# Performance work log

Measured on AMD Instinct MI355X. Metric: run time of the kernel, lower is better.

## Reference

```python
import jax, jax.numpy as jnp
import numpy as np

B, C, D, H, W = 2, 128, 16, 16, 16
NH = 4
HD = C // NH
GROUPS = 32
EPS = 1e-5


def group_norm(x, w, b):
    # x: [B, C, D, H, W]; normalize over (C/GROUPS, D, H, W) per group
    Bb, Cc = x.shape[0], x.shape[1]
    xr = x.reshape(Bb, GROUPS, -1)
    mu = xr.mean(axis=-1, keepdims=True)
    var = xr.var(axis=-1, keepdims=True)
    xn = ((xr - mu) * jax.lax.rsqrt(var + EPS)).reshape(x.shape)
    return xn * w.reshape(1, Cc, 1, 1, 1) + b.reshape(1, Cc, 1, 1, 1)


def setup_inputs() -> dict:
    key = jax.random.key(0)
    k0, k1, k2 = jax.random.split(key, 3)
    x = jax.random.normal(k0, (B, C, D, H, W), dtype=jnp.float32)
    gn_w = jnp.ones((C,), dtype=jnp.float32)
    gn_b = jnp.zeros((C,), dtype=jnp.float32)
    # 1x1x1 Conv3d weights as [out_ch, in_ch] matrices
    qkv_w = jax.random.normal(k1, (3 * C, C), dtype=jnp.float32) / np.sqrt(C).astype(np.float32)
    qkv_b = jnp.zeros((3 * C,), dtype=jnp.float32)
    out_w = jax.random.normal(k2, (C, C), dtype=jnp.float32) / np.sqrt(C).astype(np.float32)
    out_b = jnp.zeros((C,), dtype=jnp.float32)
    return {"x": x, "gn_w": gn_w, "gn_b": gn_b, "qkv_w": qkv_w, "qkv_b": qkv_b,
            "out_w": out_w, "out_b": out_b}


def reference(x, gn_w, gn_b, qkv_w, qkv_b, out_w, out_b):
    Bb, Cc, Dd, Hh, Ww = x.shape
    N = Dd * Hh * Ww
    scale = HD ** (-0.5)

    xn = group_norm(x, gn_w, gn_b)
    xf = xn.reshape(Bb, Cc, N)                              # [B, C, N]
    qkv = jnp.einsum('oc,bcn->bon', qkv_w, xf) + qkv_b[None, :, None]
    qkv = qkv.reshape(Bb, 3, NH, HD, N)
    q, k, v = qkv[:, 0], qkv[:, 1], qkv[:, 2]               # each [B, h, hd, N]

    attn = jnp.einsum('bhdn,bhdm->bhnm', q, k) * scale      # [B, h, N, N]
    attn = jax.nn.softmax(attn, axis=-1)
    o = jnp.einsum('bhnm,bhdm->bhdn', attn, v)              # [B, h, hd, N]
    o = o.reshape(Bb, Cc, N)

    y = jnp.einsum('oc,bcn->bon', out_w, o) + out_b[None, :, None]
    return y.reshape(Bb, Cc, Dd, Hh, Ww) + x
```

## Files before the change

### kernel.cpp

```cpp
#include <hip/hip_runtime.h>
#include <hip/hip_bf16.h>

#define B_ 2
#define C_ 128
#define N_ 4096
#define NH_ 4
#define HD_ 32
#define GROUPS_ 32
#define EPS_ 1e-5f
#define SCALE2_ 0.25503486f
#define NCH_ 4
#define CHKV_ 1024
#define NT_ (CHKV_ / 64)

typedef __attribute__((ext_vector_type(2))) float f32x2;
typedef __attribute__((ext_vector_type(4))) float f32x4;
typedef __attribute__((ext_vector_type(8))) short s16x8;
typedef __attribute__((ext_vector_type(2))) unsigned int u32x2;
typedef __attribute__((ext_vector_type(4))) unsigned int u32x4;
typedef unsigned short u16;
typedef unsigned int u32;

static __device__ __forceinline__ u32 cvtpk_bf16(float lo, float hi) {
  u32 r;
  asm("v_cvt_pk_bf16_f32 %0, %1, %2" : "=v"(r) : "v"(lo), "v"(hi));
  return r;
}
static __device__ __forceinline__ float fexp2(float x) {
  float r;
  asm("v_exp_f32 %0, %1" : "=v"(r) : "v"(x));
  return r;
}
static __device__ __forceinline__ float bflo(u32 w) { return __uint_as_float(w << 16); }
static __device__ __forceinline__ float bfhi(u32 w) { return __uint_as_float(w & 0xffff0000u); }

__global__ __launch_bounds__(256) void k_groupnorm(
    const float* __restrict__ x, const float* __restrict__ gw,
    const float* __restrict__ gb, u16* __restrict__ xn) {
  const int blk = blockIdx.x;
  const int tid = threadIdx.x;
  const size_t base = (size_t)blk * (4 * N_);
  const f32x4* x4 = (const f32x4*)(x + base);
  float s = 0.f, ss = 0.f;
  for (int i = tid; i < 4096; i += 256) {
    f32x4 v = x4[i];
    s  += v.x + v.y + v.z + v.w;
    ss += v.x*v.x + v.y*v.y + v.z*v.z + v.w*v.w;
  }
  for (int off = 32; off; off >>= 1) {
    s  += __shfl_down(s, off);
    ss += __shfl_down(ss, off);
  }
  __shared__ float red[2][4];
  __shared__ float mv[2];
  const int wid = tid >> 6;
  if ((tid & 63) == 0) { red[0][wid] = s; red[1][wid] = ss; }
  __syncthreads();
  if (tid == 0) {
    float S = red[0][0]+red[0][1]+red[0][2]+red[0][3];
    float Q = red[1][0]+red[1][1]+red[1][2]+red[1][3];
    float mu  = S * (1.f/16384.f);
    float var = Q * (1.f/16384.f) - mu*mu;
    mv[0] = mu; mv[1] = rsqrtf(var + EPS_);
  }
  __syncthreads();
  const float mu = mv[0], rs = mv[1];
  const int gi = blk & (GROUPS_ - 1);
  u32x2* xn2 = (u32x2*)(xn + base);
  for (int i = tid; i < 4096; i += 256) {
    const int c = gi*4 + (i >> 10);
    const float a  = gw[c] * rs;
    const float b2 = gb[c] - mu * a;
    f32x4 v = x4[i];
    f32x4 r = v * a + b2;
    u32x2 p = { cvtpk_bf16(r.x, r.y), cvtpk_bf16(r.z, r.w) };
    xn2[i] = p;
  }
}

__global__ __launch_bounds__(256) void k_gemm_qkv(
    const u16* __restrict__ xn, const float* __restrict__ w,
    const float* __restrict__ bias, u16* __restrict__ qkvb,
    u16* __restrict__ Kt) {
  const int tid = threadIdx.x;
  const int n0 = blockIdx.x * 512 + tid * 2;
  const int o0 = blockIdx.y * 8;
  const int b  = blockIdx.z;
  const u16* xb = xn + (size_t)b * C_ * N_;
  const float* wp = w + (size_t)o0 * C_;
  float ax[8] = {0,0,0,0,0,0,0,0};
  float ay[8] = {0,0,0,0,0,0,0,0};
  #pragma unroll 4
  for (int c = 0; c < C_; ++c) {
    const u32 wv = *(const u32*)(xb + (size_t)c * N_ + n0);
    const float x0 = bflo(wv), x1 = bfhi(wv);
    #pragma unroll
    for (int i = 0; i < 8; ++i) {
      const float wi = wp[(size_t)i * C_ + c];
      ax[i] += x0 * wi;
      ay[i] += x1 * wi;
    }
  }
  #pragma unroll
  for (int i = 0; i < 8; ++i) {
    const float bi = bias[o0 + i];
    ax[i] += bi; ay[i] += bi;
  }
  if (o0 < 128) {
    u16* op = qkvb + ((size_t)b * 384 + o0) * N_ + n0;
    #pragma unroll
    for (int i = 0; i < 8; ++i)
      *(u32*)(op + (size_t)i * N_) = cvtpk_bf16(ax[i] * SCALE2_, ay[i] * SCALE2_);
  } else if (o0 < 256) {
    const int h  = (o0 - 128) >> 5;
    const int d8 = (o0 - 128) & 31;
    u16* kb = Kt + (size_t)(b * NH_ + h) * N_ * HD_ + d8;
    u32x4 pk0 = { cvtpk_bf16(ax[0], ax[1]), cvtpk_bf16(ax[2], ax[3]),
                  cvtpk_bf16(ax[4], ax[5]), cvtpk_bf16(ax[6], ax[7]) };
    u32x4 pk1 = { cvtpk_bf16(ay[0], ay[1]), cvtpk_bf16(ay[2], ay[3]),
                  cvtpk_bf16(ay[4], ay[5]), cvtpk_bf16(ay[6], ay[7]) };
    *(u32x4*)(kb + (size_t)n0 * HD_)       = pk0;
    *(u32x4*)(kb + (size_t)(n0 + 1) * HD_) = pk1;
  } else {
    u16* op = qkvb + ((size_t)b * 384 + o0) * N_ + n0;
    #pragma unroll
    for (int i = 0; i < 8; ++i)
      *(u32*)(op + (size_t)i * N_) = cvtpk_bf16(ax[i], ay[i]);
  }
}

__global__ __launch_bounds__(256) void k_attn(
    const u16* __restrict__ qkvb, const u16* __restrict__ Kt,
    float* __restrict__ Opart, float* __restrict__ Lpart) {
  __shared__ u16 Kl[64 * 32];
  __shared__ u16 Vl[32 * 72];
  const int b = blockIdx.z, h = blockIdx.y;
  const int qt = blockIdx.x & 31, ch = blockIdx.x >> 5;
  const int tid = threadIdx.x;
  const int wid = tid >> 6, lane = tid & 63;
  const int g = lane >> 4, lq = lane & 15;
  const int q0 = qt * 128 + wid * 16;
  const int kv0 = ch * CHKV_;

  const u16* qb = qkvb + ((size_t)b * 384 + h * HD_) * N_;
  s16x8 qfA, qfB;
  #pragma unroll
  for (int j = 0; j < 8; ++j) {
    qfA[j] = (short)qb[(size_t)(8*g + j) * N_ + q0 + lq];
    qfB[j] = (short)qb[(size_t)(8*g + j) * N_ + q0 + 64 + lq];
  }

  const u16* ktb = Kt + (size_t)(b * NH_ + h) * N_ * HD_;
  const u16* vbb = qkvb + ((size_t)b * 384 + 256 + h * HD_) * N_;
  const int pi = ((lq >> 2) << 3) + (lq & 3);

  const u16* kst = ktb + (size_t)kv0 * HD_ + tid * 8;
  const int vrow = tid >> 3;
  const int vcol = (tid & 7) * 8;
  const u16* vst = vbb + (size_t)vrow * N_ + kv0 + vcol;
  u16* kdst = Kl + ((tid * 8) ^ (((tid >> 5) & 3) * 8));
  u16* vdst = Vl + vrow * 72 + vcol;

  const int xsw  = (pi >> 3) & 3;
  const int slot = 8 * (g ^ xsw);
  const int ka0 = (pi)      * 32 + slot;
  const int ka1 = (pi + 4)  * 32 + slot;
  const int ka2 = (pi + 32) * 32 + slot;
  const int ka3 = (pi + 36) * 32 + slot;
  const int va0 = lq * 72 + 8*g;
  const int va1 = (lq + 16) * 72 + 8*g;

  const short one_bf = (short)0x3F80;
  const s16x8 onesB = {one_bf, one_bf, one_bf, one_bf,
                       one_bf, one_bf, one_bf, one_bf};

  f32x4 oa0A = {0.f,0.f,0.f,0.f}, oa1A = oa0A, oLA = oa0A;
  f32x4 oa0B = oa0A, oa1B = oa0A, oLB = oa0A;

  {
    s16x8 kr = *(const s16x8*)(kst);
    s16x8 vr = *(const s16x8*)(vst);
    *(s16x8*)(kdst) = kr;
    *(s16x8*)(vdst) = vr;
  }
  __syncthreads();

  for (int tt = 0; tt < NT_; ++tt) {
    const int tn = (tt + 1 < NT_) ? (tt + 1) : (NT_ - 1);
    s16x8 kr = *(const s16x8*)(kst + (size_t)tn * 64 * HD_);
    s16x8 vr = *(const s16x8*)(vst + (size_t)tn * 64);

    const s16x8 ck0 = *(const s16x8*)(Kl + ka0);
    const s16x8 ck1 = *(const s16x8*)(Kl + ka1);
    const s16x8 ck2 = *(const s16x8*)(Kl + ka2);
    const s16x8 ck3 = *(const s16x8*)(Kl + ka3);
    const s16x8 cv0 = *(const s16x8*)(Vl + va0);
    const s16x8 cv1 = *(const s16x8*)(Vl + va1);
    const s16x8 cv2 = *(const s16x8*)(Vl + va0 + 32);
    const s16x8 cv3 = *(const s16x8*)(Vl + va1 + 32);

    const f32x4 z = {0.f,0.f,0.f,0.f};
    {
      f32x4 s0 = __builtin_amdgcn_mfma_f32_16x16x32_bf16(ck0, qfA, z, 0, 0, 0);
      f32x4 s1 = __builtin_amdgcn_mfma_f32_16x16x32_bf16(ck1, qfA, z, 0, 0, 0);
      f32x4 s2 = __builtin_amdgcn_mfma_f32_16x16x32_bf16(ck2, qfA, z, 0, 0, 0);
      f32x4 s3 = __builtin_amdgcn_mfma_f32_16x16x32_bf16(ck3, qfA, z, 0, 0, 0);
      float p0 = fexp2(s0.x), p1 = fexp2(s0.y), p2 = fexp2(s0.z), p3 = fexp2(s0.w);
      float p4 = fexp2(s1.x), p5 = fexp2(s1.y), p6 = fexp2(s1.z), p7 = fexp2(s1.w);
      float p8 = fexp2(s2.x), p9 = fexp2(s2.y), pa_ = fexp2(s2.z), pb_ = fexp2(s2.w);
      float pc_ = fexp2(s3.x), pd_ = fexp2(s3.y), pe_ = fexp2(s3.z), pf_ = fexp2(s3.w);
      union { u32x4 u; s16x8 s; } pkA, pkB;
      pkA.u.x = cvtpk_bf16(p0, p1);   pkA.u.y = cvtpk_bf16(p2, p3);
      pkA.u.z = cvtpk_bf16(p4, p5);   pkA.u.w = cvtpk_bf16(p6, p7);
      pkB.u.x = cvtpk_bf16(p8, p9);   pkB.u.y = cvtpk_bf16(pa_, pb_);
      pkB.u.z = cvtpk_bf16(pc_, pd_); pkB.u.w = cvtpk_bf16(pe_, pf_);
      oa0A = __builtin_amdgcn_mfma_f32_16x16x32_bf16(pkA.s, cv0, oa0A, 0, 0, 0);
      oa1A = __builtin_amdgcn_mfma_f32_16x16x32_bf16(pkA.s, cv1, oa1A, 0, 0, 0);
      oLA  = __builtin_amdgcn_mfma_f32_16x16x32_bf16(pkA.s, onesB, oLA, 0, 0, 0);
      oa0A = __builtin_amdgcn_mfma_f32_16x16x32_bf16(pkB.s, cv2, oa0A, 0, 0, 0);
      oa1A = __builtin_amdgcn_mfma_f32_16x16x32_bf16(pkB.s, cv3, oa1A, 0, 0, 0);
      oLA  = __builtin_amdgcn_mfma_f32_16x16x32_bf16(pkB.s, onesB, oLA, 0, 0, 0);
    }
    {
      f32x4 s0 = __builtin_amdgcn_mfma_f32_16x16x32_bf16(ck0, qfB, z, 0, 0, 0);
      f32x4 s1 = __builtin_amdgcn_mfma_f32_16x16x32_bf16(ck1, qfB, z, 0, 0, 0);
      f32x4 s2 = __builtin_amdgcn_mfma_f32_16x16x32_bf16(ck2, qfB, z, 0, 0, 0);
      f32x4 s3 = __builtin_amdgcn_mfma_f32_16x16x32_bf16(ck3, qfB, z, 0, 0, 0);
      float p0 = fexp2(s0.x), p1 = fexp2(s0.y), p2 = fexp2(s0.z), p3 = fexp2(s0.w);
      float p4 = fexp2(s1.x), p5 = fexp2(s1.y), p6 = fexp2(s1.z), p7 = fexp2(s1.w);
      float p8 = fexp2(s2.x), p9 = fexp2(s2.y), pa_ = fexp2(s2.z), pb_ = fexp2(s2.w);
      float pc_ = fexp2(s3.x), pd_ = fexp2(s3.y), pe_ = fexp2(s3.z), pf_ = fexp2(s3.w);
      union { u32x4 u; s16x8 s; } pkA, pkB;
      pkA.u.x = cvtpk_bf16(p0, p1);   pkA.u.y = cvtpk_bf16(p2, p3);
      pkA.u.z = cvtpk_bf16(p4, p5);   pkA.u.w = cvtpk_bf16(p6, p7);
      pkB.u.x = cvtpk_bf16(p8, p9);   pkB.u.y = cvtpk_bf16(pa_, pb_);
      pkB.u.z = cvtpk_bf16(pc_, pd_); pkB.u.w = cvtpk_bf16(pe_, pf_);
      oa0B = __builtin_amdgcn_mfma_f32_16x16x32_bf16(pkA.s, cv0, oa0B, 0, 0, 0);
      oa1B = __builtin_amdgcn_mfma_f32_16x16x32_bf16(pkA.s, cv1, oa1B, 0, 0, 0);
      oLB  = __builtin_amdgcn_mfma_f32_16x16x32_bf16(pkA.s, onesB, oLB, 0, 0, 0);
      oa0B = __builtin_amdgcn_mfma_f32_16x16x32_bf16(pkB.s, cv2, oa0B, 0, 0, 0);
      oa1B = __builtin_amdgcn_mfma_f32_16x16x32_bf16(pkB.s, cv3, oa1B, 0, 0, 0);
      oLB  = __builtin_amdgcn_mfma_f32_16x16x32_bf16(pkB.s, onesB, oLB, 0, 0, 0);
    }

    __syncthreads();
    *(s16x8*)(kdst) = kr;
    *(s16x8*)(vdst) = vr;
    __syncthreads();
  }

  const int bh = b * NH_ + h;
  float* opb = Opart + ((size_t)ch * (B_ * NH_) + bh) * ((size_t)N_ * HD_);
  #pragma unroll
  for (int r = 0; r < 4; ++r) {
    const int qrow = q0 + g*4 + r;
    opb[(size_t)qrow * HD_ + lq]             = oa0A[r];
    opb[(size_t)qrow * HD_ + lq + 16]        = oa1A[r];
    opb[(size_t)(qrow + 64) * HD_ + lq]      = oa0B[r];
    opb[(size_t)(qrow + 64) * HD_ + lq + 16] = oa1B[r];
  }
  if (lq == 0) {
    float* lp = Lpart + ((size_t)ch * (B_ * NH_) + bh) * N_ + q0 + g*4;
    lp[0] = oLA[0]; lp[1] = oLA[1]; lp[2] = oLA[2]; lp[3] = oLA[3];
    lp[64] = oLB[0]; lp[65] = oLB[1]; lp[66] = oLB[2]; lp[67] = oLB[3];
  }
}

__global__ __launch_bounds__(256) void k_out(
    const float* __restrict__ Opart, const float* __restrict__ Lpart,
    const float* __restrict__ w, const float* __restrict__ bias,
    const float* __restrict__ x, float* __restrict__ y) {
  __shared__ u16 Ot[128][136];
  __shared__ float linv[NH_][128];
  const int t = threadIdx.x;
  const int n0 = blockIdx.x * 128;
  const int o0 = blockIdx.y * 16;
  const int b  = blockIdx.z;

  if (t < 128) {
    #pragma unroll
    for (int h = 0; h < NH_; ++h) {
      float s = 0.f;
      #pragma unroll
      for (int c = 0; c < NCH_; ++c)
        s += Lpart[((size_t)c * (B_ * NH_) + b * NH_ + h) * N_ + n0 + t];
      linv[h][t] = 1.0f / s;
    }
  }
  __syncthreads();

  {
    const int dd = (t & 7) * 4;
    const int nb = t >> 3;
    #pragma unroll
    for (int h = 0; h < NH_; ++h) {
      const float* ob = Opart + (size_t)(b * NH_ + h) * ((size_t)N_ * HD_)
                      + (size_t)n0 * HD_ + dd;
      #pragma unroll
      for (int p = 0; p < 4; ++p) {
        const int nn = p * 32 + nb;
        f32x4 a = {0.f,0.f,0.f,0.f};
        #pragma unroll
        for (int c = 0; c < NCH_; ++c)
          a += *(const f32x4*)(ob + (size_t)c * ((size_t)B_ * NH_ * N_ * HD_)
                                  + (size_t)nn * HD_);
        const float iv = linv[h][nn];
        a *= iv;
        Ot[32*h + dd + 0][nn] = (u16)cvtpk_bf16(a.x, a.x);
        Ot[32*h + dd + 1][nn] = (u16)cvtpk_bf16(a.y, a.y);
        Ot[32*h + dd + 2][nn] = (u16)cvtpk_bf16(a.z, a.z);
        Ot[32*h + dd + 3][nn] = (u16)cvtpk_bf16(a.w, a.w);
      }
    }
  }
  __syncthreads();

  const int n4  = (t & 31) * 4;
  const int orow = o0 + (t >> 5) * 2;
  const float* w0p = w + (size_t)orow * C_;
  const float* w1p = w0p + C_;
  f32x4 acc0 = {0.f,0.f,0.f,0.f}, acc1 = acc0;
  #pragma unroll 4
  for (int c = 0; c < C_; ++c) {
    const u32x2 ov = *(const u32x2*)(&Ot[c][n4]);
    const f32x4 xv = { bflo(ov.x), bfhi(ov.x), bflo(ov.y), bfhi(ov.y) };
    acc0 += xv * w0p[c];
    acc1 += xv * w1p[c];
  }
  const size_t yo = ((size_t)b * C_ + orow) * N_ + n0 + n4;
  const f32x4 xr0 = *(const f32x4*)(x + yo);
  const f32x4 xr1 = *(const f32x4*)(x + yo + N_);
  *(f32x4*)(y + yo)      = acc0 + bias[orow]     + xr0;
  *(f32x4*)(y + yo + N_) = acc1 + bias[orow + 1] + xr1;
}

extern "C" void kernel_launch(void* const* d_in, const int* in_sizes, int n_in,
                              void* d_out, int out_size, void* d_ws, size_t ws_size,
                              hipStream_t stream) {
  const float* x     = (const float*)d_in[0];
  const float* gn_w  = (const float*)d_in[1];
  const float* gn_b  = (const float*)d_in[2];
  const float* qkv_w = (const float*)d_in[3];
  const float* qkv_b = (const float*)d_in[4];
  const float* out_w = (const float*)d_in[5];
  const float* out_b = (const float*)d_in[6];
  float* y = (float*)d_out;

  float* ws  = (float*)d_ws;
  u16*   xn   = (u16*)ws;
  u16*   qkvb = (u16*)(ws + 524288);
  u16*   Kt   = (u16*)(ws + 2097152);
  float* Opart = ws + 2621440;
  float* Lpart = ws + 6815744;

  k_groupnorm<<<dim3(B_ * GROUPS_), 256, 0, stream>>>(x, gn_w, gn_b, xn);
  k_gemm_qkv <<<dim3(8, 48, B_),    256, 0, stream>>>(xn, qkv_w, qkv_b, qkvb, Kt);
  k_attn     <<<dim3(32 * NCH_, NH_, B_), 256, 0, stream>>>(qkvb, Kt, Opart, Lpart);
  k_out      <<<dim3(32, 8, B_),    256, 0, stream>>>(Opart, Lpart, out_w, out_b, x, y);
}
```

Before: 75.79 us.

## Split KV into more chunks, store bf16 partials, widen groupnorm and out-proj tiles

Doubles the number of KV chunks in attention (8 chunks of 512) to launch more blocks and use more CUs. Partial attention outputs are stored as bf16 instead of fp32, halving write and read traffic between attention and the output projection. Groupnorm now runs with 1024 threads per block, and the output projection computes 4 output rows per thread with half as many blocks, which improves weight reuse. In exchange, each query reduces over more partials, and bf16 rounding of those partials adds precision error.

```diff
diff --git a/kernel.cpp b/kernel.cpp
--- a/kernel.cpp
+++ b/kernel.cpp
@@ -9,8 +9,8 @@
 #define GROUPS_ 32
 #define EPS_ 1e-5f
 #define SCALE2_ 0.25503486f
-#define NCH_ 4
-#define CHKV_ 1024
+#define NCH_ 8
+#define CHKV_ 512
 #define NT_ (CHKV_ / 64)
 
 typedef __attribute__((ext_vector_type(2))) float f32x2;
@@ -33,8 +33,9 @@
 }
 static __device__ __forceinline__ float bflo(u32 w) { return __uint_as_float(w << 16); }
 static __device__ __forceinline__ float bfhi(u32 w) { return __uint_as_float(w & 0xffff0000u); }
-
-__global__ __launch_bounds__(256) void k_groupnorm(
+static __device__ __forceinline__ u16 f2bf16(float f) { return (u16)cvtpk_bf16(f, f); }
+
+__global__ __launch_bounds__(1024) void k_groupnorm(
     const float* __restrict__ x, const float* __restrict__ gw,
     const float* __restrict__ gb, u16* __restrict__ xn) {
   const int blk = blockIdx.x;
@@ -42,7 +43,8 @@
   const size_t base = (size_t)blk * (4 * N_);
   const f32x4* x4 = (const f32x4*)(x + base);
   float s = 0.f, ss = 0.f;
-  for (int i = tid; i < 4096; i += 256) {
+  #pragma unroll
+  for (int i = tid; i < 4096; i += 1024) {
     f32x4 v = x4[i];
     s  += v.x + v.y + v.z + v.w;
     ss += v.x*v.x + v.y*v.y + v.z*v.z + v.w*v.w;
@@ -51,14 +53,15 @@
     s  += __shfl_down(s, off);
     ss += __shfl_down(ss, off);
   }
-  __shared__ float red[2][4];
+  __shared__ float red[2][16];
   __shared__ float mv[2];
   const int wid = tid >> 6;
   if ((tid & 63) == 0) { red[0][wid] = s; red[1][wid] = ss; }
   __syncthreads();
   if (tid == 0) {
-    float S = red[0][0]+red[0][1]+red[0][2]+red[0][3];
-    float Q = red[1][0]+red[1][1]+red[1][2]+red[1][3];
+    float S = 0.f, Q = 0.f;
+    #pragma unroll
+    for (int i = 0; i < 16; ++i) { S += red[0][i]; Q += red[1][i]; }
     float mu  = S * (1.f/16384.f);
     float var = Q * (1.f/16384.f) - mu*mu;
     mv[0] = mu; mv[1] = rsqrtf(var + EPS_);
@@ -67,7 +70,8 @@
   const float mu = mv[0], rs = mv[1];
   const int gi = blk & (GROUPS_ - 1);
   u32x2* xn2 = (u32x2*)(xn + base);
-  for (int i = tid; i < 4096; i += 256) {
+  #pragma unroll
+  for (int i = tid; i < 4096; i += 1024) {
     const int c = gi*4 + (i >> 10);
     const float a  = gw[c] * rs;
     const float b2 = gb[c] - mu * a;
@@ -131,7 +135,7 @@
 
 __global__ __launch_bounds__(256) void k_attn(
     const u16* __restrict__ qkvb, const u16* __restrict__ Kt,
-    float* __restrict__ Opart, float* __restrict__ Lpart) {
+    u16* __restrict__ Opart, float* __restrict__ Lpart) {
   __shared__ u16 Kl[64 * 32];
   __shared__ u16 Vl[32 * 72];
   const int b = blockIdx.z, h = blockIdx.y;
@@ -146,8 +150,9 @@
   s16x8 qfA, qfB;
   #pragma unroll
   for (int j = 0; j < 8; ++j) {
-    qfA[j] = (short)qb[(size_t)(8*g + j) * N_ + q0 + lq];
-    qfB[j] = (short)qb[(size_t)(8*g + j) * N_ + q0 + 64 + lq];
+    const u16* qr = qb + (size_t)(8*g + j) * N_ + q0 + lq;
+    qfA[j] = (short)qr[0];
+    qfB[j] = (short)qr[64];
   }
 
   const u16* ktb = Kt + (size_t)(b * NH_ + h) * N_ * HD_;
@@ -250,31 +255,31 @@
   }
 
   const int bh = b * NH_ + h;
-  float* opb = Opart + ((size_t)ch * (B_ * NH_) + bh) * ((size_t)N_ * HD_);
+  u16* opb = Opart + ((size_t)ch * (B_ * NH_) + bh) * ((size_t)N_ * HD_);
   #pragma unroll
   for (int r = 0; r < 4; ++r) {
     const int qrow = q0 + g*4 + r;
-    opb[(size_t)qrow * HD_ + lq]             = oa0A[r];
-    opb[(size_t)qrow * HD_ + lq + 16]        = oa1A[r];
-    opb[(size_t)(qrow + 64) * HD_ + lq]      = oa0B[r];
-    opb[(size_t)(qrow + 64) * HD_ + lq + 16] = oa1B[r];
+    opb[(size_t)qrow * HD_ + lq]             = f2bf16(oa0A[r]);
+    opb[(size_t)qrow * HD_ + lq + 16]        = f2bf16(oa1A[r]);
+    opb[(size_t)(qrow + 64) * HD_ + lq]      = f2bf16(oa0B[r]);
+    opb[(size_t)(qrow + 64) * HD_ + lq + 16] = f2bf16(oa1B[r]);
   }
   if (lq == 0) {
     float* lp = Lpart + ((size_t)ch * (B_ * NH_) + bh) * N_ + q0 + g*4;
-    lp[0] = oLA[0]; lp[1] = oLA[1]; lp[2] = oLA[2]; lp[3] = oLA[3];
+    lp[0]  = oLA[0]; lp[1]  = oLA[1]; lp[2]  = oLA[2]; lp[3]  = oLA[3];
     lp[64] = oLB[0]; lp[65] = oLB[1]; lp[66] = oLB[2]; lp[67] = oLB[3];
   }
 }
 
 __global__ __launch_bounds__(256) void k_out(
-    const float* __restrict__ Opart, const float* __restrict__ Lpart,
+    const u16* __restrict__ Opart, const float* __restrict__ Lpart,
     const float* __restrict__ w, const float* __restrict__ bias,
     const float* __restrict__ x, float* __restrict__ y) {
   __shared__ u16 Ot[128][136];
   __shared__ float linv[NH_][128];
   const int t = threadIdx.x;
   const int n0 = blockIdx.x * 128;
-  const int o0 = blockIdx.y * 16;
+  const int o0 = blockIdx.y * 32;
   const int b  = blockIdx.z;
 
   if (t < 128) {
@@ -294,44 +299,52 @@
     const int nb = t >> 3;
     #pragma unroll
     for (int h = 0; h < NH_; ++h) {
-      const float* ob = Opart + (size_t)(b * NH_ + h) * ((size_t)N_ * HD_)
-                      + (size_t)n0 * HD_ + dd;
+      const u16* ob = Opart + (size_t)(b * NH_ + h) * ((size_t)N_ * HD_)
+                    + (size_t)n0 * HD_ + dd;
       #pragma unroll
       for (int p = 0; p < 4; ++p) {
         const int nn = p * 32 + nb;
         f32x4 a = {0.f,0.f,0.f,0.f};
         #pragma unroll
-        for (int c = 0; c < NCH_; ++c)
-          a += *(const f32x4*)(ob + (size_t)c * ((size_t)B_ * NH_ * N_ * HD_)
-                                  + (size_t)nn * HD_);
+        for (int c = 0; c < NCH_; ++c) {
+          const u32x2 ov = *(const u32x2*)(ob
+              + (size_t)c * ((size_t)B_ * NH_ * N_ * HD_) + (size_t)nn * HD_);
+          a.x += bflo(ov.x); a.y += bfhi(ov.x);
+          a.z += bflo(ov.y); a.w += bfhi(ov.y);
+        }
         const float iv = linv[h][nn];
         a *= iv;
-        Ot[32*h + dd + 0][nn] = (u16)cvtpk_bf16(a.x, a.x);
-        Ot[32*h + dd + 1][nn] = (u16)cvtpk_bf16(a.y, a.y);
-        Ot[32*h + dd + 2][nn] = (u16)cvtpk_bf16(a.z, a.z);
-        Ot[32*h + dd + 3][nn] = (u16)cvtpk_bf16(a.w, a.w);
+        Ot[32*h + dd + 0][nn] = f2bf16(a.x);
+        Ot[32*h + dd + 1][nn] = f2bf16(a.y);
+        Ot[32*h + dd + 2][nn] = f2bf16(a.z);
+        Ot[32*h + dd + 3][nn] = f2bf16(a.w);
       }
     }
   }
   __syncthreads();
 
   const int n4  = (t & 31) * 4;
-  const int orow = o0 + (t >> 5) * 2;
-  const float* w0p = w + (size_t)orow * C_;
-  const float* w1p = w0p + C_;
-  f32x4 acc0 = {0.f,0.f,0.f,0.f}, acc1 = acc0;
+  const int orow = o0 + (t >> 5) * 4;
+  const float* wp = w + (size_t)orow * C_;
+  f32x4 acc0 = {0.f,0.f,0.f,0.f}, acc1 = acc0, acc2 = acc0, acc3 = acc0;
   #pragma unroll 4
   for (int c = 0; c < C_; ++c) {
     const u32x2 ov = *(const u32x2*)(&Ot[c][n4]);
     const f32x4 xv = { bflo(ov.x), bfhi(ov.x), bflo(ov.y), bfhi(ov.y) };
-    acc0 += xv * w0p[c];
-    acc1 += xv * w1p[c];
+    acc0 += xv * wp[c];
+    acc1 += xv * wp[C_ + c];
+    acc2 += xv * wp[2*C_ + c];
+    acc3 += xv * wp[3*C_ + c];
   }
   const size_t yo = ((size_t)b * C_ + orow) * N_ + n0 + n4;
   const f32x4 xr0 = *(const f32x4*)(x + yo);
   const f32x4 xr1 = *(const f32x4*)(x + yo + N_);
-  *(f32x4*)(y + yo)      = acc0 + bias[orow]     + xr0;
-  *(f32x4*)(y + yo + N_) = acc1 + bias[orow + 1] + xr1;
+  const f32x4 xr2 = *(const f32x4*)(x + yo + 2*N_);
+  const f32x4 xr3 = *(const f32x4*)(x + yo + 3*N_);
+  *(f32x4*)(y + yo)        = acc0 + bias[orow]     + xr0;
+  *(f32x4*)(y + yo + N_)   = acc1 + bias[orow + 1] + xr1;
+  *(f32x4*)(y + yo + 2*N_) = acc2 + bias[orow + 2] + xr2;
+  *(f32x4*)(y + yo + 3*N_) = acc3 + bias[orow + 3] + xr3;
 }
 
 extern "C" void kernel_launch(void* const* d_in, const int* in_sizes, int n_in,
@@ -350,11 +363,11 @@
   u16*   xn   = (u16*)ws;
   u16*   qkvb = (u16*)(ws + 524288);
   u16*   Kt   = (u16*)(ws + 2097152);
-  float* Opart = ws + 2621440;
+  u16*   Opart = (u16*)(ws + 2621440);
   float* Lpart = ws + 6815744;
 
-  k_groupnorm<<<dim3(B_ * GROUPS_), 256, 0, stream>>>(x, gn_w, gn_b, xn);
+  k_groupnorm<<<dim3(B_ * GROUPS_), 1024, 0, stream>>>(x, gn_w, gn_b, xn);
   k_gemm_qkv <<<dim3(8, 48, B_),    256, 0, stream>>>(xn, qkv_w, qkv_b, qkvb, Kt);
   k_attn     <<<dim3(32 * NCH_, NH_, B_), 256, 0, stream>>>(qkvb, Kt, Opart, Lpart);
-  k_out      <<<dim3(32, 8, B_),    256, 0, stream>>>(Opart, Lpart, out_w, out_b, x, y);
-}
+  k_out      <<<dim3(32, 4, B_),    256, 0, stream>>>(Opart, Lpart, out_w, out_b, x, y);
+}
```

Measured after the change: 70.39 us. 7.1% less time.
